# Performance work log

Measured on AMD Instinct MI355X. Metric: run time of the kernel, lower is better.

Reference implementation:

```python
import jax, jax.numpy as jnp
import numpy as np

T, B, I, H, O = 512, 64, 1024, 1024, 1024

def setup_inputs() -> dict:
    key = jax.random.key(0)
    ks = jax.random.split(key, 6)
    return {
        'x': jax.random.normal(ks[0], (T, B, I), dtype=jnp.float32),
        'h0': jax.random.normal(ks[1], (B, H), dtype=jnp.float32),
        'w_i2h': jax.random.normal(ks[2], (H, I + H), dtype=jnp.float32) * (1.0 / np.sqrt(I + H)),
        'b_i2h': jax.random.normal(ks[3], (H,), dtype=jnp.float32) * 0.01,
        'w_h2o': jax.random.normal(ks[4], (O, H), dtype=jnp.float32) * (1.0 / np.sqrt(H)),
        'b_h2o': jax.random.normal(ks[5], (O,), dtype=jnp.float32) * 0.01,
    }

def reference(x, h0, w_i2h, b_i2h, w_h2o, b_h2o):
    # concat([x_t, h]) @ w_i2h.T  ==  x_t @ Wx.T + h @ Wh.T, with Wx = w_i2h[:, :I], Wh = w_i2h[:, I:]
    i_dim = x.shape[-1]
    wx = w_i2h[:, :i_dim]   # [H, I]
    wh = w_i2h[:, i_dim:]   # [H, H]
    # Batch the input projection over all timesteps (same math, efficient):
    xproj = jnp.einsum('tbi,hi->tbh', x, wx) + b_i2h  # [T, B, H]

    def step(h, xp):
        h_new = jnp.tanh(xp + h @ wh.T)      # [B, H]
        y_t = h_new @ w_h2o.T + b_h2o        # [B, O]
        return h_new, y_t

    _, ys = jax.lax.scan(step, h0, xproj)    # ys: [T, B, O]
    return ys
```

## Files before the change

kernel.cpp:

```cpp
#include <hip/hip_runtime.h>
#include <math.h>

typedef __attribute__((ext_vector_type(8))) short bf16x8;
typedef __attribute__((ext_vector_type(4))) int   i32x4;
typedef __attribute__((ext_vector_type(4))) float f32x4;
typedef __attribute__((ext_vector_type(4))) unsigned short u16x4;

__device__ __forceinline__ unsigned short f2bf(float x) {
  unsigned int u = __builtin_bit_cast(unsigned int, x);
  return (unsigned short)((u + 0x7fffu + ((u >> 16) & 1u)) >> 16);
}
__device__ __forceinline__ float bf2f(unsigned short h) {
  unsigned int u = ((unsigned int)h) << 16;
  return __builtin_bit_cast(float, u);
}
__device__ __forceinline__ float fast_tanh(float z) {
  float e;
  asm("v_exp_f32 %0, %1" : "=v"(e) : "v"(z * 2.8853900817779268f));
  return 1.0f - 2.0f * __builtin_amdgcn_rcpf(e + 1.0f);
}

__global__ void convert_kernel(const float* __restrict__ w_i2h,
                               const float* __restrict__ w_h2o,
                               const float* __restrict__ h0,
                               unsigned short* __restrict__ wx,
                               unsigned short* __restrict__ wh,
                               unsigned short* __restrict__ w2o,
                               unsigned short* __restrict__ hx,
                               int* __restrict__ flags) {
  int idx = blockIdx.x * 256 + threadIdx.x;
  if (idx < 256) flags[idx] = 0;
  int e = idx * 4;
  const float* src;
  unsigned short* dst;
  if (e < 2097152) {
    int row = e >> 11, col = e & 2047;
    src = w_i2h + e;
    dst = (col < 1024) ? (wx + row * 1024 + col) : (wh + row * 1024 + (col - 1024));
  } else if (e < 3145728) {
    int i = e - 2097152; src = w_h2o + i; dst = w2o + i;
  } else {
    int i = e - 3145728; src = h0 + i; dst = hx + i;
  }
  float4 v = *(const float4*)src;
  u16x4 o = {f2bf(v.x), f2bf(v.y), f2bf(v.z), f2bf(v.w)};
  *(u16x4*)dst = o;
}

template <bool AF32, bool OUTBF16>
__global__ __launch_bounds__(256) void gemm_bt(const void* __restrict__ Ap,
                                               const unsigned short* __restrict__ B,
                                               const float* __restrict__ bias,
                                               void* __restrict__ Cp,
                                               int M, int N, int K) {
  __shared__ __attribute__((aligned(16))) unsigned short lA[128 * 64];
  __shared__ __attribute__((aligned(16))) unsigned short lB[128 * 64];
  const int tid = threadIdx.x;
  const int bx = blockIdx.x & 7;
  const int by = blockIdx.x >> 3;
  const int lane = tid & 63, w = tid >> 6;
  const int g = lane >> 4, l15 = lane & 15;
  const int wm = w >> 1, wn = w & 1;

  f32x4 acc[4][4];
#pragma unroll
  for (int i = 0; i < 4; ++i)
#pragma unroll
    for (int j = 0; j < 4; ++j) acc[i][j] = (f32x4){0.f, 0.f, 0.f, 0.f};

  const int nK = K >> 6;
  for (int kt = 0; kt < nK; ++kt) {
    const int k0 = kt << 6;
#pragma unroll
    for (int i = 0; i < 4; ++i) {
      int cl = i * 256 + tid;
      int row = cl >> 3, cc = cl & 7;
      bf16x8 av;
      if (AF32) {
        const float* ap = (const float*)Ap + (size_t)(by * 128 + row) * K + k0 + cc * 8;
        float4 f0 = *(const float4*)ap;
        float4 f1 = *(const float4*)(ap + 4);
        av = (bf16x8){(short)f2bf(f0.x), (short)f2bf(f0.y), (short)f2bf(f0.z), (short)f2bf(f0.w),
                      (short)f2bf(f1.x), (short)f2bf(f1.y), (short)f2bf(f1.z), (short)f2bf(f1.w)};
      } else {
        const unsigned short* ap = (const unsigned short*)Ap + (size_t)(by * 128 + row) * K + k0 + cc * 8;
        av = *(const bf16x8*)ap;
      }
      *(bf16x8*)&lA[(row * 8 + (cc ^ (row & 7))) * 8] = av;
      const unsigned short* bp = B + (size_t)(bx * 128 + row) * K + k0 + cc * 8;
      bf16x8 bv = *(const bf16x8*)bp;
      *(bf16x8*)&lB[(row * 8 + (cc ^ (row & 7))) * 8] = bv;
    }
    __syncthreads();
#pragma unroll
    for (int kk = 0; kk < 2; ++kk) {
      bf16x8 av[4], bv[4];
#pragma unroll
      for (int mt = 0; mt < 4; ++mt) {
        int r = wm * 64 + mt * 16 + l15;
        av[mt] = *(const bf16x8*)&lA[(r * 8 + ((kk * 4 + g) ^ (r & 7))) * 8];
      }
#pragma unroll
      for (int nt = 0; nt < 4; ++nt) {
        int r = wn * 64 + nt * 16 + l15;
        bv[nt] = *(const bf16x8*)&lB[(r * 8 + ((kk * 4 + g) ^ (r & 7))) * 8];
      }
#pragma unroll
      for (int mt = 0; mt < 4; ++mt)
#pragma unroll
        for (int nt = 0; nt < 4; ++nt)
          acc[mt][nt] = __builtin_amdgcn_mfma_f32_16x16x32_bf16(av[mt], bv[nt], acc[mt][nt], 0, 0, 0);
    }
    __syncthreads();
  }
#pragma unroll
  for (int mt = 0; mt < 4; ++mt) {
    int grow = by * 128 + wm * 64 + mt * 16 + g * 4;
#pragma unroll
    for (int nt = 0; nt < 4; ++nt) {
      int col = bx * 128 + wn * 64 + nt * 16 + l15;
      float bs = bias[col];
#pragma unroll
      for (int r = 0; r < 4; ++r) {
        size_t off = (size_t)(grow + r) * N + col;
        float v = acc[mt][nt][r] + bs;
        if (OUTBF16) ((unsigned short*)Cp)[off] = f2bf(v);
        else ((float*)Cp)[off] = v;
      }
    }
  }
}

#define SCAN_BLOCKS 256
__global__ __launch_bounds__(64, 1) void rnn_scan(const unsigned short* __restrict__ xproj,
                                                  const unsigned short* __restrict__ wh,
                                                  const unsigned short* __restrict__ w2o,
                                                  const float* __restrict__ b_h2o,
                                                  float* __restrict__ y,
                                                  unsigned short* __restrict__ hx,
                                                  int* __restrict__ flags) {
  const int tid = threadIdx.x;
  const int b = blockIdx.x;
  const int jt = b >> 2, bt = b & 3;
  const int g = tid >> 4, l15 = tid & 15;
  const int j0 = jt * 16, b0 = bt * 16;

  bf16x8 wb[32], wo[32];
#pragma unroll
  for (int kk = 0; kk < 32; ++kk) {
    wb[kk] = *(const bf16x8*)(wh  + (size_t)(j0 + l15) * 1024 + kk * 32 + g * 8);
    wo[kk] = *(const bf16x8*)(w2o + (size_t)(j0 + l15) * 1024 + kk * 32 + g * 8);
  }
  const float bias_o = b_h2o[j0 + l15];

  const int* fl = flags + bt * 64 + tid;
  int* myflag = flags + bt * 64 + jt;

  for (int t = 0; t <= 512; ++t) {
    const unsigned short* hsrc = hx + (size_t)(t & 3) * 65536 + (size_t)b0 * 1024;

    float xpv[4];
    if (t < 512) {
      const unsigned short* xp = xproj + (size_t)t * 65536;
#pragma unroll
      for (int r = 0; r < 4; ++r)
        xpv[r] = bf2f(xp[(size_t)(b0 + g * 4 + r) * 1024 + j0 + l15]);
    }

    int v;
    do {
      asm volatile("global_load_dword %0, %1, off sc0 sc1\n\ts_waitcnt vmcnt(0)"
                   : "=v"(v) : "v"(fl) : "memory");
    } while (__any(v < t));

    i32x4 ha[32];
#pragma unroll
    for (int kk = 0; kk < 32; ++kk) {
      const unsigned short* p = hsrc + (size_t)l15 * 1024 + kk * 32 + g * 8;
      asm volatile("global_load_dwordx4 %0, %1, off sc0 sc1"
                   : "=v"(ha[kk]) : "v"(p) : "memory");
    }

    if (t < 512) {
      unsigned short* hdst = hx + (size_t)((t + 1) & 3) * 65536;
      f32x4 acc[4];
#pragma unroll
      for (int i = 0; i < 4; ++i) acc[i] = (f32x4){0.f, 0.f, 0.f, 0.f};

#define MFMA_GROUP(base, n)                                                     \
      asm volatile("s_waitcnt vmcnt(" #n ")" ::: "memory");                     \
      __builtin_amdgcn_sched_barrier(0);                                        \
      _Pragma("unroll")                                                         \
      for (int kk = base; kk < base + 8; ++kk)                                  \
        acc[kk & 3] = __builtin_amdgcn_mfma_f32_16x16x32_bf16(                  \
            __builtin_bit_cast(bf16x8, ha[kk]), wb[kk], acc[kk & 3], 0, 0, 0);

      MFMA_GROUP(0, 24)
      MFMA_GROUP(8, 16)
      MFMA_GROUP(16, 8)
      MFMA_GROUP(24, 0)
#undef MFMA_GROUP

      f32x4 s = (acc[0] + acc[1]) + (acc[2] + acc[3]);

#pragma unroll
      for (int r = 0; r < 4; ++r) {
        float z = s[r] + xpv[r];
        unsigned int hv = f2bf(fast_tanh(z));
        unsigned short* p = hdst + (size_t)(b0 + g * 4 + r) * 1024 + j0 + l15;
        asm volatile("global_store_short %0, %1, off sc0 sc1"
                     :: "v"(p), "v"(hv) : "memory");
      }
      asm volatile("s_waitcnt vmcnt(0)" ::: "memory");
      if (tid == 0) {
        int tv = t + 1;
        asm volatile("global_store_dword %0, %1, off sc0 sc1"
                     :: "v"(myflag), "v"(tv) : "memory");
      }
    } else {
      asm volatile("s_waitcnt vmcnt(0)" ::: "memory");
      __builtin_amdgcn_sched_barrier(0);
    }

    if (t > 0) {
      f32x4 ay[4];
#pragma unroll
      for (int i = 0; i < 4; ++i) ay[i] = (f32x4){0.f, 0.f, 0.f, 0.f};
#pragma unroll
      for (int kk = 0; kk < 32; ++kk)
        ay[kk & 3] = __builtin_amdgcn_mfma_f32_16x16x32_bf16(
            __builtin_bit_cast(bf16x8, ha[kk]), wo[kk], ay[kk & 3], 0, 0, 0);
      f32x4 sy = (ay[0] + ay[1]) + (ay[2] + ay[3]);
#pragma unroll
      for (int r = 0; r < 4; ++r)
        y[(size_t)(t - 1) * 65536 + (size_t)(b0 + g * 4 + r) * 1024 + j0 + l15] = sy[r] + bias_o;
    }
  }
}

extern "C" void kernel_launch(void* const* d_in, const int* in_sizes, int n_in,
                              void* d_out, int out_size, void* d_ws, size_t ws_size,
                              hipStream_t stream) {
  const float* x     = (const float*)d_in[0];
  const float* h0    = (const float*)d_in[1];
  const float* w_i2h = (const float*)d_in[2];
  const float* b_i2h = (const float*)d_in[3];
  const float* w_h2o = (const float*)d_in[4];
  const float* b_h2o = (const float*)d_in[5];

  char* ws = (char*)d_ws;
  unsigned short* xproj = (unsigned short*)ws;
  unsigned short* hx    = (unsigned short*)(ws + 67108864);
  int*            flags = (int*)(ws + 67108864 + 524288);
  unsigned short* wx    = (unsigned short*)(ws + 67108864 + 524288 + 4096);
  unsigned short* wh    = wx + 1024 * 1024;
  unsigned short* w2o   = wh + 1024 * 1024;
  float* y = (float*)d_out;

  convert_kernel<<<3136, 256, 0, stream>>>(w_i2h, w_h2o, h0, wx, wh, w2o, hx, flags);

  gemm_bt<true, true><<<2048, 256, 0, stream>>>((const void*)x, wx, b_i2h,
                                                (void*)xproj, 32768, 1024, 1024);

  rnn_scan<<<SCAN_BLOCKS, 64, 0, stream>>>(xproj, wh, w2o, b_h2o, y, hx, flags);
}
```

Baseline: 1.674 ms.

## Swap MFMA operands for vectorized h/y stores and pad sync flags

Swaps the MFMA A/B operands so each lane holds four consecutive hidden units rather than four batch rows. The recurrent h update then becomes one dwordx2 store, the xproj read one 8-byte load, and the output one float4 store, replacing scattered 2-byte and 4-byte accesses. Each per-block sync flag is also padded to its own 64-byte slot to avoid false sharing during polling. The flag region grows, so the workspace offsets shift.

```diff
diff --git a/kernel.cpp b/kernel.cpp
--- a/kernel.cpp
+++ b/kernel.cpp
@@ -29,7 +29,7 @@
                                unsigned short* __restrict__ hx,
                                int* __restrict__ flags) {
   int idx = blockIdx.x * 256 + threadIdx.x;
-  if (idx < 256) flags[idx] = 0;
+  if (idx < 4096) flags[idx] = 0;
   int e = idx * 4;
   const float* src;
   unsigned short* dst;
@@ -151,21 +151,19 @@
     wb[kk] = *(const bf16x8*)(wh  + (size_t)(j0 + l15) * 1024 + kk * 32 + g * 8);
     wo[kk] = *(const bf16x8*)(w2o + (size_t)(j0 + l15) * 1024 + kk * 32 + g * 8);
   }
-  const float bias_o = b_h2o[j0 + l15];
-
-  const int* fl = flags + bt * 64 + tid;
-  int* myflag = flags + bt * 64 + jt;
+  const float4 bias_o = *(const float4*)(b_h2o + j0 + g * 4);
+
+  const int* fl = flags + (bt * 64 + tid) * 16;
+  int* myflag = flags + (bt * 64 + jt) * 16;
+
+  const int pofs = (b0 + l15) * 1024 + j0 + g * 4;
 
   for (int t = 0; t <= 512; ++t) {
     const unsigned short* hsrc = hx + (size_t)(t & 3) * 65536 + (size_t)b0 * 1024;
 
-    float xpv[4];
-    if (t < 512) {
-      const unsigned short* xp = xproj + (size_t)t * 65536;
-#pragma unroll
-      for (int r = 0; r < 4; ++r)
-        xpv[r] = bf2f(xp[(size_t)(b0 + g * 4 + r) * 1024 + j0 + l15]);
-    }
+    uint2 xpc;
+    if (t < 512)
+      xpc = *(const uint2*)(xproj + (size_t)t * 65536 + pofs);
 
     int v;
     do {
@@ -193,7 +191,7 @@
       _Pragma("unroll")                                                         \
       for (int kk = base; kk < base + 8; ++kk)                                  \
         acc[kk & 3] = __builtin_amdgcn_mfma_f32_16x16x32_bf16(                  \
-            __builtin_bit_cast(bf16x8, ha[kk]), wb[kk], acc[kk & 3], 0, 0, 0);
+            wb[kk], __builtin_bit_cast(bf16x8, ha[kk]), acc[kk & 3], 0, 0, 0);
 
       MFMA_GROUP(0, 24)
       MFMA_GROUP(8, 16)
@@ -203,13 +201,19 @@
 
       f32x4 s = (acc[0] + acc[1]) + (acc[2] + acc[3]);
 
-#pragma unroll
-      for (int r = 0; r < 4; ++r) {
-        float z = s[r] + xpv[r];
-        unsigned int hv = f2bf(fast_tanh(z));
-        unsigned short* p = hdst + (size_t)(b0 + g * 4 + r) * 1024 + j0 + l15;
-        asm volatile("global_store_short %0, %1, off sc0 sc1"
-                     :: "v"(p), "v"(hv) : "memory");
+      {
+        float z0 = s[0] + bf2f((unsigned short)(xpc.x & 0xFFFF));
+        float z1 = s[1] + bf2f((unsigned short)(xpc.x >> 16));
+        float z2 = s[2] + bf2f((unsigned short)(xpc.y & 0xFFFF));
+        float z3 = s[3] + bf2f((unsigned short)(xpc.y >> 16));
+        unsigned int v01 = (unsigned int)f2bf(fast_tanh(z0)) |
+                           ((unsigned int)f2bf(fast_tanh(z1)) << 16);
+        unsigned int v23 = (unsigned int)f2bf(fast_tanh(z2)) |
+                           ((unsigned int)f2bf(fast_tanh(z3)) << 16);
+        uint2 dvec = {v01, v23};
+        unsigned short* p = hdst + pofs;
+        asm volatile("global_store_dwordx2 %0, %1, off sc0 sc1"
+                     :: "v"(p), "v"(dvec) : "memory");
       }
       asm volatile("s_waitcnt vmcnt(0)" ::: "memory");
       if (tid == 0) {
@@ -229,11 +233,10 @@
 #pragma unroll
       for (int kk = 0; kk < 32; ++kk)
         ay[kk & 3] = __builtin_amdgcn_mfma_f32_16x16x32_bf16(
-            __builtin_bit_cast(bf16x8, ha[kk]), wo[kk], ay[kk & 3], 0, 0, 0);
+            wo[kk], __builtin_bit_cast(bf16x8, ha[kk]), ay[kk & 3], 0, 0, 0);
       f32x4 sy = (ay[0] + ay[1]) + (ay[2] + ay[3]);
-#pragma unroll
-      for (int r = 0; r < 4; ++r)
-        y[(size_t)(t - 1) * 65536 + (size_t)(b0 + g * 4 + r) * 1024 + j0 + l15] = sy[r] + bias_o;
+      sy[0] += bias_o.x; sy[1] += bias_o.y; sy[2] += bias_o.z; sy[3] += bias_o.w;
+      *(f32x4*)(y + (size_t)(t - 1) * 65536 + pofs) = sy;
     }
   }
 }
@@ -252,7 +255,7 @@
   unsigned short* xproj = (unsigned short*)ws;
   unsigned short* hx    = (unsigned short*)(ws + 67108864);
   int*            flags = (int*)(ws + 67108864 + 524288);
-  unsigned short* wx    = (unsigned short*)(ws + 67108864 + 524288 + 4096);
+  unsigned short* wx    = (unsigned short*)(ws + 67108864 + 524288 + 16384);
   unsigned short* wh    = wx + 1024 * 1024;
   unsigned short* w2o   = wh + 1024 * 1024;
   float* y = (float*)d_out;
```

Result: faster. 1.537 ms (-8.1%).
